# Kernel tuning notes

Measured on AMD Instinct MI355X. Metric: run time of the kernel, lower is better.

Reference implementation:

```python
import jax, jax.numpy as jnp
import numpy as np
from jax import lax

B, T, C, F_IN = 32, 2048, 64, 8
CONV_F, ATT_D, HID, N_CLS = 32, 32, 128, 4


def layer_norm(x, scale, bias, eps=1e-6):
    mu = jnp.mean(x, axis=-1, keepdims=True)
    var = jnp.mean(jnp.square(x - mu), axis=-1, keepdims=True)
    return (x - mu) * lax.rsqrt(var + eps) * scale + bias


def setup_inputs() -> dict:
    key = jax.random.key(0)
    ks = jax.random.split(key, 12)
    s = lambda *sh: 1.0 / np.sqrt(sh[-2] if len(sh) > 1 else sh[-1])
    inp = {
        "X": jax.random.normal(ks[0], (B, T, C, F_IN), jnp.float32),
        "conv_w": jax.random.normal(ks[1], (5, 1, F_IN, CONV_F), jnp.float32) * 0.1,
        "conv_b": jnp.zeros((CONV_F,), jnp.float32),
        "ln1_s": jnp.ones((CONV_F,), jnp.float32),
        "ln1_b": jnp.zeros((CONV_F,), jnp.float32),
        "q_w": jax.random.normal(ks[2], (CONV_F, ATT_D), jnp.float32) * s(CONV_F, ATT_D),
        "q_b": jnp.zeros((ATT_D,), jnp.float32),
        "k_w": jax.random.normal(ks[3], (CONV_F, ATT_D), jnp.float32) * s(CONV_F, ATT_D),
        "k_b": jnp.zeros((ATT_D,), jnp.float32),
        "ca_w": jax.random.normal(ks[4], (C, C), jnp.float32) * s(C, C),
        "ca_b": jnp.zeros((C,), jnp.float32),
        "mix_w": jax.random.normal(ks[5], (C * CONV_F, HID), jnp.float32) * s(C * CONV_F, HID),
        "mix_b": jnp.zeros((HID,), jnp.float32),
        "ln2_s": jnp.ones((HID,), jnp.float32),
        "ln2_b": jnp.zeros((HID,), jnp.float32),
        "decay_logit": jnp.full((1, HID), 2.0, jnp.float32),
        "fc_w": jax.random.normal(ks[6], (HID, HID), jnp.float32) * s(HID, HID),
        "fc_b": jnp.zeros((HID,), jnp.float32),
        "out_w": jax.random.normal(ks[7], (HID, N_CLS), jnp.float32) * s(HID, N_CLS),
        "out_b": jnp.zeros((N_CLS,), jnp.float32),
        "train": False,
    }
    return inp


def reference(X, conv_w, conv_b, ln1_s, ln1_b, q_w, q_b, k_w, k_b, ca_w, ca_b,
              mix_w, mix_b, ln2_s, ln2_b, decay_logit, fc_w, fc_b, out_w, out_b, train):
    # eval mode (train=False): no input noise, dropout is identity
    # conv: (B,T,C,F_in) -> (B,T/2,C,32), SAME padding, stride (2,1)
    Xc = lax.conv_general_dilated(X, conv_w, window_strides=(2, 1), padding='SAME',
                                  dimension_numbers=('NHWC', 'HWIO', 'NHWC')) + conv_b
    Xc = jax.nn.relu(Xc)
    Xc = layer_norm(Xc, ln1_s, ln1_b)

    # dynamic graph attention over channel axis
    x_spat = jnp.mean(Xc, axis=1)                         # (B,C,32)
    q = x_spat @ q_w + q_b
    k = x_spat @ k_w + k_b
    adj = jax.nn.softmax(jnp.einsum('bcf,bdf->bcd', q, k) / jnp.sqrt(jnp.float32(ATT_D)), axis=-1)
    Xg = jnp.einsum('bcd,btdf->btcf', adj, Xc)            # (B,T2,C,32)

    # channel gating
    ca = jax.nn.sigmoid(jnp.mean(Xc, axis=(1, 3)) @ ca_w + ca_b)  # (B,C)
    Xr = Xg * ca[:, None, :, None] + Xc

    b, t2 = Xr.shape[0], Xr.shape[1]
    Xf = Xr.reshape(b, t2, -1)                            # (B,T2,2048)
    Xm = jax.nn.relu(Xf @ mix_w + mix_b)
    Xm = layer_norm(Xm, ln2_s, ln2_b)                     # (B,T2,128)

    # LIF spiking recurrence over time
    decay = jax.nn.sigmoid(decay_logit)                   # (1,128)

    def step(mem, xt):
        mem = mem * decay + xt
        spk = (mem - 0.5 > 0).astype(mem.dtype)
        mem = mem - spk * 0.5
        return mem, spk

    _, spk_seq = lax.scan(step, jnp.zeros((b, HID), Xm.dtype), jnp.swapaxes(Xm, 0, 1))
    spk_seq = jnp.swapaxes(spk_seq, 0, 1)                 # (B,T2,128)

    feat = jnp.mean(spk_seq, axis=1)                      # (B,128)
    feat = jax.nn.relu(feat @ fc_w + fc_b)
    logits = feat @ out_w + out_b
    return logits, jnp.mean(spk_seq)
```

## Files before the change

kernel.cpp:

```cpp
#include <hip/hip_runtime.h>
#include <math.h>

#define B_    32
#define T_    2048
#define T2_   1024
#define C_    64
#define FI_   8
#define FO_   32
#define K_    2048
#define H_    128

typedef unsigned short u16;
typedef short bf16x8 __attribute__((ext_vector_type(8)));
typedef float f32x4 __attribute__((ext_vector_type(4)));

#define OFF_WTH  ((size_t)67108864)
#define OFF_WTL  ((size_t)71303168)
#define OFF_XSP  ((size_t)75497472)
#define OFF_A    ((size_t)77594624)
#define OFF_XM   ((size_t)77725696)

__device__ __forceinline__ float bft(float x) {
  unsigned u = __float_as_uint(x);
  u = (u + 0x7fffu + ((u >> 16) & 1u)) & 0xffff0000u;
  return __uint_as_float(u);
}
__device__ __forceinline__ unsigned bfpack(float a, float b) {
  unsigned ua = __float_as_uint(a); ua = (ua + 0x7fffu + ((ua >> 16) & 1u)) >> 16;
  unsigned ub = __float_as_uint(b); ub = (ub + 0x7fffu + ((ub >> 16) & 1u)) & 0xffff0000u;
  return ua | ub;
}
__device__ __forceinline__ unsigned cvtpk(float a, float b) {
  unsigned r;
  asm("v_cvt_pk_bf16_f32 %0, %1, %2" : "=v"(r) : "v"(a), "v"(b));
  return r;
}
__device__ __forceinline__ bf16x8 packhi(const float4& x0, const float4& x1) {
  uint4 hv = make_uint4(cvtpk(x0.x, x0.y), cvtpk(x0.z, x0.w),
                        cvtpk(x1.x, x1.y), cvtpk(x1.z, x1.w));
  return *(bf16x8*)&hv;
}
__device__ __forceinline__ void pack8(const float4& x0, const float4& x1,
                                      bf16x8& h, bf16x8& l) {
  float v[8] = {x0.x, x0.y, x0.z, x0.w, x1.x, x1.y, x1.z, x1.w};
  unsigned hu[4], lu[4];
#pragma unroll
  for (int p = 0; p < 4; ++p) {
    const float a = v[2*p], b2 = v[2*p+1];
    const unsigned ph = cvtpk(a, b2);
    hu[p] = ph;
    const float fa_ = __uint_as_float(ph << 16);
    const float fb_ = __uint_as_float(ph & 0xffff0000u);
    lu[p] = cvtpk(a - fa_, b2 - fb_);
  }
  uint4 hv = make_uint4(hu[0], hu[1], hu[2], hu[3]);
  uint4 lv = make_uint4(lu[0], lu[1], lu[2], lu[3]);
  h = *(bf16x8*)&hv; l = *(bf16x8*)&lv;
}

__device__ __forceinline__ void glds16(const u16* g, u16* l) {
  auto gp = reinterpret_cast<const __attribute__((address_space(1))) unsigned int*>(
      reinterpret_cast<uintptr_t>(g));
  auto lp = reinterpret_cast<__attribute__((address_space(3))) unsigned int*>(
      reinterpret_cast<uintptr_t>(l));
  __builtin_amdgcn_global_load_lds(gp, lp, 16, 0, 0);
}

__global__ __launch_bounds__(256, 3) void k1_conv_ln(
    const float* __restrict__ X, const float* __restrict__ Wc,
    const float* __restrict__ bc, const float* __restrict__ g1,
    const float* __restrict__ be1, float* __restrict__ xsp)
{
  __shared__ float xred[4][1056];
  const int tid = threadIdx.x;
  const int w = tid >> 6, lane = tid & 63;
  const int q = lane >> 4, cl = lane & 15;
  const int chalf = w & 1, rng = w >> 1;
  const int b = blockIdx.y, tile = blockIdx.x;
  const int cbase = chalf * 32;

  bf16x8 Wh[2][2], Wl[2][2];
#pragma unroll
  for (int s = 0; s < 2; ++s)
#pragma unroll
    for (int mt = 0; mt < 2; ++mt) {
      const int f = mt * 16 + cl;
      float x8[8];
#pragma unroll
      for (int j = 0; j < 8; ++j) {
        float wv;
        if (s == 0) {
          wv = Wc[(q * 8 + j) * 32 + f];
        } else {
          wv = 0.f;
          if (q == 0) wv = Wc[(32 + j) * 32 + f];
          if (q == 1 && j == 0) wv = bc[f];
        }
        x8[j] = wv;
      }
      unsigned hu[4], lu[4];
#pragma unroll
      for (int p = 0; p < 4; ++p) {
        const float a0 = x8[2*p], a1 = x8[2*p+1];
        hu[p] = bfpack(a0, a1);
        lu[p] = bfpack(a0 - bft(a0), a1 - bft(a1));
      }
      uint4 hv = make_uint4(hu[0], hu[1], hu[2], hu[3]);
      uint4 lv = make_uint4(lu[0], lu[1], lu[2], lu[3]);
      Wh[s][mt] = *(bf16x8*)&hv;
      Wl[s][mt] = *(bf16x8*)&lv;
    }

  float g1r[2][4], be1r[2][4];
#pragma unroll
  for (int mt = 0; mt < 2; ++mt)
#pragma unroll
    for (int r = 0; r < 4; ++r) {
      const int f = mt * 16 + 4 * q + r;
      g1r[mt][r] = g1[f];
      be1r[mt][r] = be1[f];
    }

  float sacc[2][2][4];
#pragma unroll
  for (int mt = 0; mt < 2; ++mt)
#pragma unroll
    for (int nt = 0; nt < 2; ++nt)
#pragma unroll
      for (int r = 0; r < 4; ++r) sacc[mt][nt][r] = 0.f;

  const float* Xb = X + (size_t)b * T_ * C_ * FI_;
  const float4 z4f = make_float4(0.f, 0.f, 0.f, 0.f);

#pragma unroll 2
  for (int it = 0; it < 16; ++it) {
    const int t2 = tile * 32 + rng * 16 + it;
    f32x4 acc[2][2];
#pragma unroll
    for (int mt = 0; mt < 2; ++mt)
#pragma unroll
      for (int nt = 0; nt < 2; ++nt) acc[mt][nt] = (f32x4){0.f,0.f,0.f,0.f};

#pragma unroll
    for (int nt = 0; nt < 2; ++nt) {
      const int c = cbase + nt * 16 + cl;
      const float* Xbc = Xb + (size_t)c * FI_;
      bf16x8 Bh0, Bh1;
      {
        const int row = 2 * t2 + q - 1;
        const bool ok = (row >= 0) && (row < T_);
        float4 xa = z4f, xb2 = z4f;
        if (ok) {
          const float* p = Xbc + (size_t)row * (C_ * FI_);
          xa = *(const float4*)p; xb2 = *(const float4*)(p + 4);
        }
        Bh0 = packhi(xa, xb2);
      }
      {
        const int row = 2 * t2 + 3;
        const bool ok = (q == 0) && (row < T_);
        float4 xa = z4f, xb2 = z4f;
        if (ok) {
          const float* p = Xbc + (size_t)row * (C_ * FI_);
          xa = *(const float4*)p; xb2 = *(const float4*)(p + 4);
        }
        Bh1 = packhi(xa, xb2);
        if (q == 1) Bh1[0] = (short)0x3F80;
      }
#pragma unroll
      for (int mt = 0; mt < 2; ++mt) {
        acc[mt][nt] = __builtin_amdgcn_mfma_f32_16x16x32_bf16(Wh[0][mt], Bh0, acc[mt][nt], 0, 0, 0);
        acc[mt][nt] = __builtin_amdgcn_mfma_f32_16x16x32_bf16(Wl[0][mt], Bh0, acc[mt][nt], 0, 0, 0);
        acc[mt][nt] = __builtin_amdgcn_mfma_f32_16x16x32_bf16(Wh[1][mt], Bh1, acc[mt][nt], 0, 0, 0);
        acc[mt][nt] = __builtin_amdgcn_mfma_f32_16x16x32_bf16(Wl[1][mt], Bh1, acc[mt][nt], 0, 0, 0);
      }
    }

#pragma unroll
    for (int nt = 0; nt < 2; ++nt) {
      float v[2][4];
      float s1 = 0.f, s2 = 0.f;
#pragma unroll
      for (int mt = 0; mt < 2; ++mt)
#pragma unroll
        for (int r = 0; r < 4; ++r) {
          const float vv = fmaxf(acc[mt][nt][r], 0.f);
          v[mt][r] = vv; s1 += vv; s2 = fmaf(vv, vv, s2);
        }
      s1 += __shfl_xor(s1, 16); s2 += __shfl_xor(s2, 16);
      s1 += __shfl_xor(s1, 32); s2 += __shfl_xor(s2, 32);
      const float mu = s1 * (1.f / 32.f);
      const float var = s2 * (1.f / 32.f) - mu * mu;
      const float rs = rsqrtf(var + 1e-6f);
#pragma unroll
      for (int mt = 0; mt < 2; ++mt)
#pragma unroll
        for (int r = 0; r < 4; ++r)
          sacc[mt][nt][r] += (v[mt][r] - mu) * rs * g1r[mt][r] + be1r[mt][r];
    }
  }

#pragma unroll
  for (int mt = 0; mt < 2; ++mt)
#pragma unroll
    for (int nt = 0; nt < 2; ++nt)
#pragma unroll
      for (int r = 0; r < 4; ++r)
        xred[w][(nt * 16 + cl) * 33 + mt * 16 + 4 * q + r] = sacc[mt][nt][r];
  __syncthreads();
  if (w < 2) {
#pragma unroll
    for (int mt = 0; mt < 2; ++mt)
#pragma unroll
      for (int nt = 0; nt < 2; ++nt)
#pragma unroll
        for (int r = 0; r < 4; ++r) {
          const int idx = (nt * 16 + cl) * 33 + mt * 16 + 4 * q + r;
          const float vv = xred[w][idx] + xred[w + 2][idx];
          xsp[((size_t)b * 32 + tile) * 2048 +
              (size_t)(w * 32 + nt * 16 + cl) * 32 + mt * 16 + 4 * q + r] = vv;
        }
  }
}

__global__ __launch_bounds__(256) void k2_graph(
    const float* __restrict__ xsp, const float* __restrict__ qw,
    const float* __restrict__ qb, const float* __restrict__ kw,
    const float* __restrict__ kb, const float* __restrict__ caw,
    const float* __restrict__ cab, float* __restrict__ Aout)
{
  __shared__ float xs[64 * 32];
  __shared__ float qs[64][32];
  __shared__ float ks[64][32];
  __shared__ float sc[64][64];
  __shared__ float cain[64];
  __shared__ float cav[64];
  const int tid = threadIdx.x;
  const int b = blockIdx.x;

  for (int idx = tid; idx < 2048; idx += 256) {
    float s = 0.f;
    for (int p = 0; p < 32; ++p) s += xsp[((size_t)b * 32 + p) * 2048 + idx];
    xs[idx] = s * (1.f / (float)T2_);
  }
  __syncthreads();

  if (tid < 64) {
    float s = 0.f;
#pragma unroll
    for (int f = 0; f < 32; ++f) s += xs[tid * 32 + f];
    cain[tid] = s * (1.f / 32.f);
  }
  {
    const int cc = tid >> 2, part = tid & 3;
    float aq[8], ak[8];
#pragma unroll
    for (int j = 0; j < 8; ++j) { aq[j] = qb[part*8+j]; ak[j] = kb[part*8+j]; }
    for (int f = 0; f < 32; ++f) {
      const float xv = xs[cc * 32 + f];
#pragma unroll
      for (int j = 0; j < 8; ++j) {
        aq[j] = fmaf(xv, qw[f * 32 + part*8+j], aq[j]);
        ak[j] = fmaf(xv, kw[f * 32 + part*8+j], ak[j]);
      }
    }
#pragma unroll
    for (int j = 0; j < 8; ++j) { qs[cc][part*8+j] = aq[j]; ks[cc][part*8+j] = ak[j]; }
  }
  __syncthreads();
  {
    const int cc = tid >> 2, part = tid & 3;
    for (int dd = part * 16; dd < part * 16 + 16; ++dd) {
      float s = 0.f;
#pragma unroll
      for (int e = 0; e < 32; ++e) s = fmaf(qs[cc][e], ks[dd][e], s);
      sc[cc][dd] = s * 0.1767766953f;
    }
  }
  __syncthreads();
  if (tid < 64) {
    const int cc = tid;
    float m = -1e30f;
    for (int d = 0; d < 64; ++d) m = fmaxf(m, sc[cc][d]);
    float sum = 0.f;
    for (int d = 0; d < 64; ++d) { float e = expf(sc[cc][d] - m); sc[cc][d] = e; sum += e; }
    const float inv = 1.f / sum;
    for (int d = 0; d < 64; ++d) sc[cc][d] *= inv;
    float a = cab[cc];
    for (int d = 0; d < 64; ++d) a = fmaf(cain[d], caw[d * 64 + cc], a);
    cav[cc] = 1.f / (1.f + expf(-a));
  }
  __syncthreads();
  for (int idx = tid; idx < 4096; idx += 256) {
    const int cc = idx >> 6, dd = idx & 63;
    Aout[(size_t)b * 4096 + idx] = cav[cc] * sc[cc][dd] + (cc == dd ? 1.f : 0.f);
  }
}

__global__ __launch_bounds__(256) void k3_weff(
    const float* __restrict__ Aout, const float* __restrict__ mixw,
    u16* __restrict__ Wth, u16* __restrict__ Wtl)
{
  __shared__ float Ap[4096];
  __shared__ float Ms[2048];
  const int tid = threadIdx.x;
  const int b = blockIdx.x >> 5, ht = blockIdx.x & 31;
  const int d = tid & 63, hl = tid >> 6;
  const int h0 = ht * 4;
  const float* Ab = Aout + (size_t)b * 4096;
#pragma unroll
  for (int l = 0; l < 16; ++l) Ap[tid + 256 * l] = Ab[tid + 256 * l];

  float acc[32];
#pragma unroll
  for (int j = 0; j < 32; ++j) acc[j] = 0.f;

  for (int c0 = 0; c0 < 64; c0 += 16) {
    __syncthreads();
    {
      const int i0 = tid * 8;
#pragma unroll
      for (int qd = 0; qd < 2; ++qd) {
        const int i = i0 + qd * 4;
        const int cc = i >> 7, f = (i >> 2) & 31;
        const float4 v = *(const float4*)&mixw[((size_t)((c0+cc)*32 + f))*128 + h0];
        float* mp = &Ms[cc * 128 + f];
        mp[0] = v.x; mp[32] = v.y; mp[64] = v.z; mp[96] = v.w;
      }
    }
    __syncthreads();
#pragma unroll 4
    for (int cc = 0; cc < 16; ++cc) {
      const float a = Ap[(c0 + cc) * 64 + d];
      const float* mrow = &Ms[cc * 128 + hl * 32];
#pragma unroll
      for (int fq = 0; fq < 8; ++fq) {
        const f32x4 m = *(const f32x4*)&mrow[fq * 4];
        acc[fq*4+0] = fmaf(a, m[0], acc[fq*4+0]);
        acc[fq*4+1] = fmaf(a, m[1], acc[fq*4+1]);
        acc[fq*4+2] = fmaf(a, m[2], acc[fq*4+2]);
        acc[fq*4+3] = fmaf(a, m[3], acc[fq*4+3]);
      }
    }
  }

  const int h = h0 + hl;
  const size_t obase = ((size_t)(b * 64 + d) * 128 + h) * 32;
#pragma unroll
  for (int g = 0; g < 4; ++g) {
    unsigned hq[4], lq[4];
#pragma unroll
    for (int jj = 0; jj < 4; ++jj) {
      const float ya = acc[8*g + 2*jj], yb = acc[8*g + 2*jj + 1];
      const float ha = bft(ya), hb = bft(yb);
      hq[jj] = (__float_as_uint(ha) >> 16) | (__float_as_uint(hb) & 0xffff0000u);
      lq[jj] = bfpack(ya - ha, yb - hb);
    }
    const int pg = (g ^ hl ^ (ht & 3)) * 8;
    *(uint4*)(Wth + obase + pg) = make_uint4(hq[0], hq[1], hq[2], hq[3]);
    *(uint4*)(Wtl + obase + pg) = make_uint4(lq[0], lq[1], lq[2], lq[3]);
  }
}

__global__ __launch_bounds__(256, 2) void k4_fused(
    const float* __restrict__ X, const float* __restrict__ Wc,
    const float* __restrict__ bc, const float* __restrict__ g1,
    const float* __restrict__ be1,
    const u16* __restrict__ Bgh, const u16* __restrict__ Bgl,
    const float* __restrict__ mixb, const float* __restrict__ g2,
    const float* __restrict__ be2, float* __restrict__ Xm)
{
  __shared__ __align__(16) u16 lds[26624];
  __shared__ float part[64 * 8];
  __shared__ float murs[128];

  const int tid = threadIdx.x;
  const int w = tid >> 6, lane = tid & 63;
  const int q = lane >> 4, cl = lane & 15;
  const int x = blockIdx.x;
  const int swz = (x & 7) * 64 + (x >> 3);
  const int b = swz >> 4, mt = swz & 15;
  const int m0 = mt * 64;

  bf16x8 Wh[2][2], Wl[2][2];
#pragma unroll
  for (int s = 0; s < 2; ++s)
#pragma unroll
    for (int m2 = 0; m2 < 2; ++m2) {
      const int f = m2 * 16 + cl;
      float x8[8];
#pragma unroll
      for (int j = 0; j < 8; ++j) {
        float wv;
        if (s == 0) {
          wv = Wc[(q * 8 + j) * 32 + f];
        } else {
          wv = 0.f;
          if (q == 0) wv = Wc[(32 + j) * 32 + f];
          if (q == 1 && j == 0) wv = bc[f];
        }
        x8[j] = wv;
      }
      unsigned hu[4], lu[4];
#pragma unroll
      for (int p = 0; p < 4; ++p) {
        const float a0 = x8[2*p], a1 = x8[2*p+1];
        hu[p] = bfpack(a0, a1);
        lu[p] = bfpack(a0 - bft(a0), a1 - bft(a1));
      }
      uint4 hv = make_uint4(hu[0], hu[1], hu[2], hu[3]);
      uint4 lv = make_uint4(lu[0], lu[1], lu[2], lu[3]);
      Wh[s][m2] = *(bf16x8*)&hv;
      Wl[s][m2] = *(bf16x8*)&lv;
    }
  float g1r[2][4], be1r[2][4];
#pragma unroll
  for (int m2 = 0; m2 < 2; ++m2)
#pragma unroll
    for (int r = 0; r < 4; ++r) {
      const int f = m2 * 16 + 4 * q + r;
      g1r[m2][r] = g1[f];
      be1r[m2][r] = be1[f];
    }

  f32x4 acc[4][2];
#pragma unroll
  for (int i = 0; i < 4; ++i)
#pragma unroll
    for (int j = 0; j < 2; ++j) acc[i][j] = (f32x4){0.f, 0.f, 0.f, 0.f};

  const int lrow = lane >> 2, lg = lane & 3;
  const size_t brow0 = (size_t)b * 262144 + (size_t)(w * 16 + lrow) * 32 + lg * 8;
  const int dA = w * 512;
  const int faA = cl * 40 + ((q ^ (cl & 3)) * 8);
  const int faB = cl * 32 + ((q ^ (cl & 3) ^ (cl >> 2)) * 8);
  const float* Xb = X + (size_t)b * T_ * (C_ * FI_);
  const int t2 = m0 + w * 16 + cl;
  const int t2loc = w * 16 + cl;

  const int r0 = 2 * t2 + q - 1, r1 = 2 * t2 + 3;
  const bool ok0 = (r0 >= 0) && (r0 < T_);
  const bool ok1 = (q == 0) && (r1 < T_);
  const float* rp0 = Xb + (size_t)(ok0 ? r0 : 0) * (C_ * FI_);
  const float* rp1 = Xb + (size_t)(ok1 ? r1 : 0) * (C_ * FI_);
  const float4 z4f = make_float4(0.f, 0.f, 0.f, 0.f);

  float4 A0a, A1a, B0a, B1a;
  float4 A0b, A1b, B0b, B1b;

  auto LOADX = [&](float4& X0, float4& X1, float4& Y0, float4& Y1, int c) {
    X0 = z4f; X1 = z4f; Y0 = z4f; Y1 = z4f;
    if (ok0) { const float* p = rp0 + c * FI_; X0 = *(const float4*)p; X1 = *(const float4*)(p + 4); }
    if (ok1) { const float* p = rp1 + c * FI_; Y0 = *(const float4*)p; Y1 = *(const float4*)(p + 4); }
  };

  auto CONV = [&](const float4& X0, const float4& X1,
                  const float4& Y0, const float4& Y1, int nb) {
    bf16x8 Bh0, Bl0, Bh1, Bl1;
    pack8(X0, X1, Bh0, Bl0);
    pack8(Y0, Y1, Bh1, Bl1);
    if (q == 1) Bh1[0] = (short)0x3F80;
    f32x4 ca0 = (f32x4){0.f,0.f,0.f,0.f}, ca1 = ca0;
    ca0 = __builtin_amdgcn_mfma_f32_16x16x32_bf16(Wh[0][0], Bh0, ca0, 0, 0, 0);
    ca1 = __builtin_amdgcn_mfma_f32_16x16x32_bf16(Wh[0][1], Bh0, ca1, 0, 0, 0);
    ca0 = __builtin_amdgcn_mfma_f32_16x16x32_bf16(Wh[0][0], Bl0, ca0, 0, 0, 0);
    ca1 = __builtin_amdgcn_mfma_f32_16x16x32_bf16(Wh[0][1], Bl0, ca1, 0, 0, 0);
    ca0 = __builtin_amdgcn_mfma_f32_16x16x32_bf16(Wl[0][0], Bh0, ca0, 0, 0, 0);
    ca1 = __builtin_amdgcn_mfma_f32_16x16x32_bf16(Wl[0][1], Bh0, ca1, 0, 0, 0);
    ca0 = __builtin_amdgcn_mfma_f32_16x16x32_bf16(Wh[1][0], Bh1, ca0, 0, 0, 0);
    ca1 = __builtin_amdgcn_mfma_f32_16x16x32_bf16(Wh[1][1], Bh1, ca1, 0, 0, 0);
    ca0 = __builtin_amdgcn_mfma_f32_16x16x32_bf16(Wh[1][0], Bl1, ca0, 0, 0, 0);
    ca1 = __builtin_amdgcn_mfma_f32_16x16x32_bf16(Wh[1][1], Bl1, ca1, 0, 0, 0);
    ca0 = __builtin_amdgcn_mfma_f32_16x16x32_bf16(Wl[1][0], Bh1, ca0, 0, 0, 0);
    ca1 = __builtin_amdgcn_mfma_f32_16x16x32_bf16(Wl[1][1], Bh1, ca1, 0, 0, 0);
    float v[2][4];
    float s1 = 0.f, s2 = 0.f;
#pragma unroll
    for (int r = 0; r < 4; ++r) {
      float vv = fmaxf(ca0[r], 0.f); v[0][r] = vv; s1 += vv; s2 = fmaf(vv, vv, s2);
      vv = fmaxf(ca1[r], 0.f);       v[1][r] = vv; s1 += vv; s2 = fmaf(vv, vv, s2);
    }
    s1 += __shfl_xor(s1, 16); s2 += __shfl_xor(s2, 16);
    s1 += __shfl_xor(s1, 32); s2 += __shfl_xor(s2, 32);
    const float mu = s1 * (1.f / 32.f);
    const float var = s2 * (1.f / 32.f) - mu * mu;
    const float rs = rsqrtf(var + 1e-6f);
    const int ab = nb * 5120;
#pragma unroll
    for (int m2 = 0; m2 < 2; ++m2) {
      float y[4];
#pragma unroll
      for (int r = 0; r < 4; ++r)
        y[r] = (v[m2][r] - mu) * rs * g1r[m2][r] + be1r[m2][r];
      const unsigned h0 = cvtpk(y[0], y[1]);
      const unsigned h1 = cvtpk(y[2], y[3]);
      const float f00 = __uint_as_float(h0 << 16);
      const float f01 = __uint_as_float(h0 & 0xffff0000u);
      const float f10 = __uint_as_float(h1 << 16);
      const float f11 = __uint_as_float(h1 & 0xffff0000u);
      const unsigned l0 = cvtpk(y[0] - f00, y[1] - f01);
      const unsigned l1 = cvtpk(y[2] - f10, y[3] - f11);
      const int phys = (2 * m2 + (q >> 1)) ^ (cl & 3);
      const int off = ab + t2loc * 40 + phys * 8 + (q & 1) * 4;
      *(uint2*)&lds[off] = make_uint2(h0, h1);
      *(uint2*)&lds[off + 2560] = make_uint2(l0, l1);
    }
  };

#define STAGE_B(kt, nb) do {                                                 \
    const int bb_ = 10240 + (nb) * 8192;                                     \
    glds16(Bgh + brow0 + (size_t)(kt) * 4096,        &lds[bb_ + dA]);        \
    glds16(Bgh + brow0 + (size_t)(kt) * 4096 + 2048, &lds[bb_ + 2048 + dA]); \
    glds16(Bgl + brow0 + (size_t)(kt) * 4096,        &lds[bb_ + 4096 + dA]); \
    glds16(Bgl + brow0 + (size_t)(kt) * 4096 + 2048, &lds[bb_ + 6144 + dA]); \
  } while (0)

  auto GEMM = [&](int nb) {
    const int ab = nb * 5120, bb = 10240 + nb * 8192;
    bf16x8 ah[4], al[4], bh[2], bl[2];
#pragma unroll
    for (int mf = 0; mf < 4; ++mf) {
      ah[mf] = *(const bf16x8*)&lds[ab + mf * 640 + faA];
      al[mf] = *(const bf16x8*)&lds[ab + 2560 + mf * 640 + faA];
    }
#pragma unroll
    for (int nf = 0; nf < 2; ++nf) {
      bh[nf] = *(const bf16x8*)&lds[bb + w * 1024 + nf * 512 + faB];
      bl[nf] = *(const bf16x8*)&lds[bb + 4096 + w * 1024 + nf * 512 + faB];
    }
#pragma unroll
    for (int mf = 0; mf < 4; ++mf)
#pragma unroll
      for (int nf = 0; nf < 2; ++nf) {
        acc[mf][nf] = __builtin_amdgcn_mfma_f32_16x16x32_bf16(ah[mf], bh[nf], acc[mf][nf], 0, 0, 0);
        acc[mf][nf] = __builtin_amdgcn_mfma_f32_16x16x32_bf16(ah[mf], bl[nf], acc[mf][nf], 0, 0, 0);
        acc[mf][nf] = __builtin_amdgcn_mfma_f32_16x16x32_bf16(al[mf], bh[nf], acc[mf][nf], 0, 0, 0);
      }
  };

  LOADX(A0a, A1a, B0a, B1a, 0);
  STAGE_B(0, 0);
  LOADX(A0b, A1b, B0b, B1b, 1);
  CONV(A0a, A1a, B0a, B1a, 0);
  __syncthreads();

  for (int kt = 0; kt < 64; kt += 2) {
    if (kt + 2 < 64) LOADX(A0a, A1a, B0a, B1a, kt + 2);
    STAGE_B(kt + 1, 1);
    GEMM(0);
    CONV(A0b, A1b, B0b, B1b, 1);
    __syncthreads();
    if (kt + 3 < 64) LOADX(A0b, A1b, B0b, B1b, kt + 3);
    if (kt + 2 < 64) STAGE_B(kt + 2, 0);
    GEMM(1);
    if (kt + 2 < 64) CONV(A0a, A1a, B0a, B1a, 0);
    __syncthreads();
  }
#undef STAGE_B

  const int c0 = w * 32 + (lane & 15);
  const float bias0 = mixb[c0], bias1 = mixb[c0 + 16];
#pragma unroll
  for (int mf = 0; mf < 4; ++mf)
#pragma unroll
    for (int r = 0; r < 4; ++r) {
      float v0 = fmaxf(acc[mf][0][r] + bias0, 0.f);
      float v1 = fmaxf(acc[mf][1][r] + bias1, 0.f);
      acc[mf][0][r] = v0; acc[mf][1][r] = v1;
      float s1 = v0 + v1, s2 = v0 * v0 + v1 * v1;
      s1 += __shfl_xor(s1, 1);  s2 += __shfl_xor(s2, 1);
      s1 += __shfl_xor(s1, 2);  s2 += __shfl_xor(s2, 2);
      s1 += __shfl_xor(s1, 4);  s2 += __shfl_xor(s2, 4);
      s1 += __shfl_xor(s1, 8);  s2 += __shfl_xor(s2, 8);
      if ((lane & 15) == 0) {
        const int row = mf * 16 + (lane >> 4) * 4 + r;
        part[row * 8 + w * 2] = s1;
        part[row * 8 + w * 2 + 1] = s2;
      }
    }
  __syncthreads();
  if (tid < 64) {
    const float s1 = part[tid*8] + part[tid*8+2] + part[tid*8+4] + part[tid*8+6];
    const float s2 = part[tid*8+1] + part[tid*8+3] + part[tid*8+5] + part[tid*8+7];
    const float mu = s1 * (1.f / 128.f);
    const float var = s2 * (1.f / 128.f) - mu * mu;
    murs[tid * 2] = mu;
    murs[tid * 2 + 1] = rsqrtf(var + 1e-6f);
  }
  __syncthreads();
  const float g20 = g2[c0], g21 = g2[c0 + 16];
  const float b20 = be2[c0], b21 = be2[c0 + 16];
#pragma unroll
  for (int mf = 0; mf < 4; ++mf)
#pragma unroll
    for (int r = 0; r < 4; ++r) {
      const int row = mf * 16 + (lane >> 4) * 4 + r;
      const float mu = murs[row * 2], rs = murs[row * 2 + 1];
      float* op = Xm + (size_t)(b * 1024 + m0 + row) * 128;
      op[c0]      = (acc[mf][0][r] - mu) * rs * g20 + b20;
      op[c0 + 16] = (acc[mf][1][r] - mu) * rs * g21 + b21;
    }
}

__global__ __launch_bounds__(64) void k5_lif(
    const float* __restrict__ Xm, const float* __restrict__ dl,
    float* __restrict__ fs)
{
  const int id = blockIdx.x * 64 + threadIdx.x;
  const int b = id >> 7, h = id & 127;
  const float decay = 1.f / (1.f + expf(-dl[h]));
  float mem = 0.f, cnt = 0.f;
  const float* p = Xm + (size_t)b * T2_ * H_ + h;
#pragma unroll 16
  for (int t = 0; t < T2_; ++t) {
    const float xv = p[(size_t)t * H_];
    mem = fmaf(mem, decay, xv);
    const float sp = ((mem - 0.5f) > 0.f) ? 1.f : 0.f;
    cnt += sp;
    mem -= 0.5f * sp;
  }
  fs[b * H_ + h] = cnt;
}

__global__ __launch_bounds__(256) void k6_head(
    const float* __restrict__ fs, const float* __restrict__ fcw,
    const float* __restrict__ fcb, const float* __restrict__ ow,
    const float* __restrict__ ob, float* __restrict__ out)
{
  __shared__ float f[32 * 128];
  __shared__ float fr[32 * 128];
  __shared__ float red[256];
  const int tid = threadIdx.x;
  float tot = 0.f;
  for (int idx = tid; idx < 4096; idx += 256) {
    const float v = fs[idx];
    f[idx] = v * (1.f / (float)T2_);
    tot += v;
  }
  red[tid] = tot;
  __syncthreads();
  for (int s = 128; s > 0; s >>= 1) {
    if (tid < s) red[tid] += red[tid + s];
    __syncthreads();
  }
  {
    const int bb = tid >> 3, og = tid & 7;
    float a[16];
#pragma unroll
    for (int j = 0; j < 16; ++j) a[j] = fcb[og * 16 + j];
    for (int hh = 0; hh < 128; ++hh) {
      const float fv = f[bb * 128 + hh];
#pragma unroll
      for (int j = 0; j < 16; ++j)
        a[j] = fmaf(fv, fcw[hh * 128 + og * 16 + j], a[j]);
    }
#pragma unroll
    for (int j = 0; j < 16; ++j) fr[bb * 128 + og * 16 + j] = fmaxf(a[j], 0.f);
  }
  __syncthreads();
  if (tid < 128) {
    const int bb = tid >> 2, cls = tid & 3;
    float a = ob[cls];
    for (int o = 0; o < 128; ++o) a = fmaf(fr[bb * 128 + o], ow[o * 4 + cls], a);
    out[bb * 4 + cls] = a;
  }
  if (tid == 0) out[128] = red[0] * (1.f / (4096.f * 1024.f));
}

extern "C" void kernel_launch(void* const* d_in, const int* in_sizes, int n_in,
                              void* d_out, int out_size, void* d_ws, size_t ws_size,
                              hipStream_t stream) {
  const float* X     = (const float*)d_in[0];
  const float* convw = (const float*)d_in[1];
  const float* convb = (const float*)d_in[2];
  const float* ln1s  = (const float*)d_in[3];
  const float* ln1b  = (const float*)d_in[4];
  const float* qw    = (const float*)d_in[5];
  const float* qb    = (const float*)d_in[6];
  const float* kw    = (const float*)d_in[7];
  const float* kb    = (const float*)d_in[8];
  const float* caw   = (const float*)d_in[9];
  const float* cab   = (const float*)d_in[10];
  const float* mixw  = (const float*)d_in[11];
  const float* mixb  = (const float*)d_in[12];
  const float* ln2s  = (const float*)d_in[13];
  const float* ln2b  = (const float*)d_in[14];
  const float* dl    = (const float*)d_in[15];
  const float* fcw   = (const float*)d_in[16];
  const float* fcb   = (const float*)d_in[17];
  const float* outw  = (const float*)d_in[18];
  const float* outb  = (const float*)d_in[19];

  float* ws  = (float*)d_ws;
  u16* Wth   = (u16*)(ws + OFF_WTH);
  u16* Wtl   = (u16*)(ws + OFF_WTL);
  float* xsp = ws + OFF_XSP;
  float* Aou = ws + OFF_A;
  float* Xm  = ws + OFF_XM;
  float* fs  = ws + OFF_A;

  dim3 g1(32, 32);
  k1_conv_ln<<<g1, 256, 0, stream>>>(X, convw, convb, ln1s, ln1b, xsp);
  k2_graph<<<32, 256, 0, stream>>>(xsp, qw, qb, kw, kb, caw, cab, Aou);
  k3_weff<<<1024, 256, 0, stream>>>(Aou, mixw, Wth, Wtl);
  k4_fused<<<512, 256, 0, stream>>>(X, convw, convb, ln1s, ln1b,
                                    Wth, Wtl, mixb, ln2s, ln2b, Xm);
  k5_lif<<<64, 64, 0, stream>>>(Xm, dl, fs);
  k6_head<<<1, 256, 0, stream>>>(fs, fcw, fcb, outw, outb, (float*)d_out);
}
```

Before: 307.4 us.

## Drop low bf16 split of effective weights and raise occupancy in conv and GEMM kernels

The effective mixing weights were stored as a hi+lo bf16 pair, and the GEMM ran three MFMAs per fragment; now only the hi part is kept and two MFMAs are issued. This halves the weight-staging loads and B-tile LDS, which lets k4 shrink shared memory and raise its occupancy hint from 2 to 4. Separately, k1 uses twice as many time tiles with half the work each and a higher occupancy hint, and the A-tile LDS swizzle is removed. The reduced weight precision risks accuracy near the spike threshold, and the unswizzled A-tile layout may cause LDS bank conflicts.

```diff
diff --git a/kernel.cpp b/kernel.cpp
--- a/kernel.cpp
+++ b/kernel.cpp
@@ -14,9 +14,8 @@
 typedef short bf16x8 __attribute__((ext_vector_type(8)));
 typedef float f32x4 __attribute__((ext_vector_type(4)));
 
+#define OFF_XSP  ((size_t)0)
 #define OFF_WTH  ((size_t)67108864)
-#define OFF_WTL  ((size_t)71303168)
-#define OFF_XSP  ((size_t)75497472)
 #define OFF_A    ((size_t)77594624)
 #define OFF_XM   ((size_t)77725696)
 
@@ -66,7 +65,7 @@
   __builtin_amdgcn_global_load_lds(gp, lp, 16, 0, 0);
 }
 
-__global__ __launch_bounds__(256, 3) void k1_conv_ln(
+__global__ __launch_bounds__(256, 6) void k1_conv_ln(
     const float* __restrict__ X, const float* __restrict__ Wc,
     const float* __restrict__ bc, const float* __restrict__ g1,
     const float* __restrict__ be1, float* __restrict__ xsp)
@@ -133,8 +132,8 @@
   const float4 z4f = make_float4(0.f, 0.f, 0.f, 0.f);
 
 #pragma unroll 2
-  for (int it = 0; it < 16; ++it) {
-    const int t2 = tile * 32 + rng * 16 + it;
+  for (int it = 0; it < 8; ++it) {
+    const int t2 = tile * 16 + rng * 8 + it;
     f32x4 acc[2][2];
 #pragma unroll
     for (int mt = 0; mt < 2; ++mt)
@@ -217,7 +216,7 @@
         for (int r = 0; r < 4; ++r) {
           const int idx = (nt * 16 + cl) * 33 + mt * 16 + 4 * q + r;
           const float vv = xred[w][idx] + xred[w + 2][idx];
-          xsp[((size_t)b * 32 + tile) * 2048 +
+          xsp[((size_t)b * 64 + tile) * 2048 +
               (size_t)(w * 32 + nt * 16 + cl) * 32 + mt * 16 + 4 * q + r] = vv;
         }
   }
@@ -240,7 +239,7 @@
 
   for (int idx = tid; idx < 2048; idx += 256) {
     float s = 0.f;
-    for (int p = 0; p < 32; ++p) s += xsp[((size_t)b * 32 + p) * 2048 + idx];
+    for (int p = 0; p < 64; ++p) s += xsp[((size_t)b * 64 + p) * 2048 + idx];
     xs[idx] = s * (1.f / (float)T2_);
   }
   __syncthreads();
@@ -299,7 +298,7 @@
 
 __global__ __launch_bounds__(256) void k3_weff(
     const float* __restrict__ Aout, const float* __restrict__ mixw,
-    u16* __restrict__ Wth, u16* __restrict__ Wtl)
+    u16* __restrict__ Wth)
 {
   __shared__ float Ap[4096];
   __shared__ float Ms[2048];
@@ -348,29 +347,24 @@
   const size_t obase = ((size_t)(b * 64 + d) * 128 + h) * 32;
 #pragma unroll
   for (int g = 0; g < 4; ++g) {
-    unsigned hq[4], lq[4];
-#pragma unroll
-    for (int jj = 0; jj < 4; ++jj) {
-      const float ya = acc[8*g + 2*jj], yb = acc[8*g + 2*jj + 1];
-      const float ha = bft(ya), hb = bft(yb);
-      hq[jj] = (__float_as_uint(ha) >> 16) | (__float_as_uint(hb) & 0xffff0000u);
-      lq[jj] = bfpack(ya - ha, yb - hb);
-    }
+    unsigned hq[4];
+#pragma unroll
+    for (int jj = 0; jj < 4; ++jj)
+      hq[jj] = bfpack(acc[8*g + 2*jj], acc[8*g + 2*jj + 1]);
     const int pg = (g ^ hl ^ (ht & 3)) * 8;
     *(uint4*)(Wth + obase + pg) = make_uint4(hq[0], hq[1], hq[2], hq[3]);
-    *(uint4*)(Wtl + obase + pg) = make_uint4(lq[0], lq[1], lq[2], lq[3]);
-  }
-}
-
-__global__ __launch_bounds__(256, 2) void k4_fused(
+  }
+}
+
+__global__ __launch_bounds__(256, 4) void k4_fused(
     const float* __restrict__ X, const float* __restrict__ Wc,
     const float* __restrict__ bc, const float* __restrict__ g1,
     const float* __restrict__ be1,
-    const u16* __restrict__ Bgh, const u16* __restrict__ Bgl,
+    const u16* __restrict__ Bgh,
     const float* __restrict__ mixb, const float* __restrict__ g2,
     const float* __restrict__ be2, float* __restrict__ Xm)
 {
-  __shared__ __align__(16) u16 lds[26624];
+  __shared__ __align__(16) u16 lds[18432];
   __shared__ float part[64 * 8];
   __shared__ float murs[128];
 
@@ -432,7 +426,7 @@
   const int lrow = lane >> 2, lg = lane & 3;
   const size_t brow0 = (size_t)b * 262144 + (size_t)(w * 16 + lrow) * 32 + lg * 8;
   const int dA = w * 512;
-  const int faA = cl * 40 + ((q ^ (cl & 3)) * 8);
+  const int faA = cl * 40 + q * 8;
   const int faB = cl * 32 + ((q ^ (cl & 3) ^ (cl >> 2)) * 8);
   const float* Xb = X + (size_t)b * T_ * (C_ * FI_);
   const int t2 = m0 + w * 16 + cl;
@@ -500,7 +494,7 @@
       const float f11 = __uint_as_float(h1 & 0xffff0000u);
       const unsigned l0 = cvtpk(y[0] - f00, y[1] - f01);
       const unsigned l1 = cvtpk(y[2] - f10, y[3] - f11);
-      const int phys = (2 * m2 + (q >> 1)) ^ (cl & 3);
+      const int phys = 2 * m2 + (q >> 1);
       const int off = ab + t2loc * 40 + phys * 8 + (q & 1) * 4;
       *(uint2*)&lds[off] = make_uint2(h0, h1);
       *(uint2*)&lds[off + 2560] = make_uint2(l0, l1);
@@ -508,32 +502,27 @@
   };
 
 #define STAGE_B(kt, nb) do {                                                 \
-    const int bb_ = 10240 + (nb) * 8192;                                     \
+    const int bb_ = 10240 + (nb) * 4096;                                     \
     glds16(Bgh + brow0 + (size_t)(kt) * 4096,        &lds[bb_ + dA]);        \
     glds16(Bgh + brow0 + (size_t)(kt) * 4096 + 2048, &lds[bb_ + 2048 + dA]); \
-    glds16(Bgl + brow0 + (size_t)(kt) * 4096,        &lds[bb_ + 4096 + dA]); \
-    glds16(Bgl + brow0 + (size_t)(kt) * 4096 + 2048, &lds[bb_ + 6144 + dA]); \
   } while (0)
 
   auto GEMM = [&](int nb) {
-    const int ab = nb * 5120, bb = 10240 + nb * 8192;
-    bf16x8 ah[4], al[4], bh[2], bl[2];
+    const int ab = nb * 5120, bb = 10240 + nb * 4096;
+    bf16x8 ah[4], al[4], bh[2];
 #pragma unroll
     for (int mf = 0; mf < 4; ++mf) {
       ah[mf] = *(const bf16x8*)&lds[ab + mf * 640 + faA];
       al[mf] = *(const bf16x8*)&lds[ab + 2560 + mf * 640 + faA];
     }
 #pragma unroll
-    for (int nf = 0; nf < 2; ++nf) {
+    for (int nf = 0; nf < 2; ++nf)
       bh[nf] = *(const bf16x8*)&lds[bb + w * 1024 + nf * 512 + faB];
-      bl[nf] = *(const bf16x8*)&lds[bb + 4096 + w * 1024 + nf * 512 + faB];
-    }
 #pragma unroll
     for (int mf = 0; mf < 4; ++mf)
 #pragma unroll
       for (int nf = 0; nf < 2; ++nf) {
         acc[mf][nf] = __builtin_amdgcn_mfma_f32_16x16x32_bf16(ah[mf], bh[nf], acc[mf][nf], 0, 0, 0);
-        acc[mf][nf] = __builtin_amdgcn_mfma_f32_16x16x32_bf16(ah[mf], bl[nf], acc[mf][nf], 0, 0, 0);
         acc[mf][nf] = __builtin_amdgcn_mfma_f32_16x16x32_bf16(al[mf], bh[nf], acc[mf][nf], 0, 0, 0);
       }
   };
@@ -692,19 +681,18 @@
   const float* outb  = (const float*)d_in[19];
 
   float* ws  = (float*)d_ws;
+  float* xsp = ws + OFF_XSP;
   u16* Wth   = (u16*)(ws + OFF_WTH);
-  u16* Wtl   = (u16*)(ws + OFF_WTL);
-  float* xsp = ws + OFF_XSP;
   float* Aou = ws + OFF_A;
   float* Xm  = ws + OFF_XM;
   float* fs  = ws + OFF_A;
 
-  dim3 g1(32, 32);
+  dim3 g1(64, 32);
   k1_conv_ln<<<g1, 256, 0, stream>>>(X, convw, convb, ln1s, ln1b, xsp);
   k2_graph<<<32, 256, 0, stream>>>(xsp, qw, qb, kw, kb, caw, cab, Aou);
-  k3_weff<<<1024, 256, 0, stream>>>(Aou, mixw, Wth, Wtl);
+  k3_weff<<<1024, 256, 0, stream>>>(Aou, mixw, Wth);
   k4_fused<<<512, 256, 0, stream>>>(X, convw, convb, ln1s, ln1b,
-                                    Wth, Wtl, mixb, ln2s, ln2b, Xm);
+                                    Wth, mixb, ln2s, ln2b, Xm);
   k5_lif<<<64, 64, 0, stream>>>(Xm, dl, fs);
   k6_head<<<1, 256, 0, stream>>>(fs, fcw, fcb, outw, outb, (float*)d_out);
 }
```

Result: slower. 602.3 us (+95.9%).
